# Optimization experiments

Measured on AMD Instinct MI355X. Metric: run time of the kernel, lower is better.

Reference implementation:

```python
import jax, jax.numpy as jnp
import numpy as np

G, B, DEG, BATCH = 4000, 8, 32, 128  # genes, per-gene layersize, off-diag blocks/gene, batch


def setup_inputs() -> dict:
    key = jax.random.key(0)
    rng = np.random.default_rng(0)
    # block structure: DEG off-diagonal PPI blocks per gene + reflexive diagonal
    src = np.repeat(np.arange(G, dtype=np.int32), DEG)
    off = 1 + rng.integers(0, G - 1, size=G * DEG)          # never 0 -> off-diagonal
    dst = ((src.astype(np.int64) + off) % G).astype(np.int32)
    diag = np.arange(G, dtype=np.int32)
    block_in = jnp.asarray(np.concatenate([src, diag]))      # [N] = [G*DEG + G]
    block_out = jnp.asarray(np.concatenate([dst, diag]))     # [N]
    n_blocks = G * DEG + G
    k1, k2 = jax.random.split(key)
    x = jax.random.normal(k1, (BATCH, G * B), dtype=jnp.float32)
    w = jax.random.normal(k2, (n_blocks, B, B), dtype=jnp.float32) * 0.05
    return {"x": x, "w": w, "block_in": block_in, "block_out": block_out}


def reference(x, w, block_in, block_out):
    batch, d = x.shape
    n_blocks, b, _ = w.shape
    g = d // b
    xb = x.reshape(batch, g, b)
    xin = xb[:, block_in, :]                        # [batch, N, b] irregular gather
    contrib = jnp.einsum('bni,nio->nbo', xin, w)    # [N, batch, b] tiny per-block GEMMs
    out = jax.ops.segment_sum(contrib, block_out, num_segments=g)  # [g, batch, b] scatter-add
    out = jnp.transpose(out, (1, 0, 2)).reshape(batch, d)
    # activation_function is identity (default lambda x: x); residual=True
    return out + x
```

## Files before the change

kernel.cpp:

```cpp
#include <hip/hip_runtime.h>
#include <hip/hip_bf16.h>

#define G      4000
#define DEG    32
#define BATCH  128
#define D      32000
#define NBLK   132000
#define ZBLK   NBLK
#define CAP    96

typedef __attribute__((ext_vector_type(8))) short bf16x8;
typedef __attribute__((ext_vector_type(4))) float f32x4;

__device__ inline unsigned bf16rne(float f) {
    unsigned u = __float_as_uint(f);
    return (u + 0x7fffu + ((u >> 16) & 1u)) >> 16;
}

__global__ void zero_cnt_kernel(int* cnt) {
    int i = blockIdx.x * 256 + threadIdx.x;
    if (i < G) cnt[i] = 0;
}

#define NB_BUILD 516
#define NB_TR    1000
#define NB_WP    4126

__global__ __launch_bounds__(256) void prep_kernel(const float* __restrict__ x,
                                                   const float* __restrict__ w,
                                                   const int* __restrict__ block_in,
                                                   const int* __restrict__ block_out,
                                                   int* __restrict__ cnt,
                                                   int2* __restrict__ pairs,
                                                   unsigned short* __restrict__ xgb,
                                                   unsigned short* __restrict__ wtb) {
    __shared__ float tile[32][132];
    const int bid = blockIdx.x;
    const int t   = threadIdx.x;

    if (bid < NB_BUILD) {
        int n = bid * 256 + t;
        if (n < NBLK) {
            int dst = block_out[n];
            int src = block_in[n];
            int pos = atomicAdd(&cnt[dst], 1);
            if (pos < CAP) pairs[dst * CAP + pos] = make_int2(n, src);
        }
    } else if (bid < NB_BUILD + NB_TR) {
        int id = bid - NB_BUILD;
        int c0 = (id % 250) * 128;
        int b0 = (id / 250) * 32;
#pragma unroll
        for (int it = 0; it < 4; ++it) {
            int l  = it * 1024 + t * 4;
            int br = l >> 7;
            int c  = l & 127;
            float4 v = *(const float4*)(x + (size_t)(b0 + br) * D + c0 + c);
            *(float4*)&tile[br][c] = v;
        }
        __syncthreads();
#pragma unroll
        for (int it = 0; it < 2; ++it) {
            int idx = it * 256 + t;
            int gl  = idx >> 5;
            int bl  = idx & 31;
            float4 v0 = *(const float4*)&tile[bl][gl * 8];
            float4 v1 = *(const float4*)&tile[bl][gl * 8 + 4];
            uint4 p;
            p.x = bf16rne(v0.x) | (bf16rne(v0.y) << 16);
            p.y = bf16rne(v0.z) | (bf16rne(v0.w) << 16);
            p.z = bf16rne(v1.x) | (bf16rne(v1.y) << 16);
            p.w = bf16rne(v1.z) | (bf16rne(v1.w) << 16);
            int gidx = (c0 >> 3) + gl;
            *(uint4*)(xgb + ((size_t)gidx * BATCH + b0 + bl) * 8) = p;
        }
    } else {
        int idx = (bid - (NB_BUILD + NB_TR)) * 256 + t;
        if (idx < (NBLK + 1) * 8) {
            int n = idx >> 3;
            int o = idx & 7;
            float v[8];
            if (n < NBLK) {
#pragma unroll
                for (int i = 0; i < 8; ++i) v[i] = w[(size_t)n * 64 + i * 8 + o];
            } else {
#pragma unroll
                for (int i = 0; i < 8; ++i) v[i] = 0.0f;
            }
            uint4 p;
            p.x = bf16rne(v[0]) | (bf16rne(v[1]) << 16);
            p.y = bf16rne(v[2]) | (bf16rne(v[3]) << 16);
            p.z = bf16rne(v[4]) | (bf16rne(v[5]) << 16);
            p.w = bf16rne(v[6]) | (bf16rne(v[7]) << 16);
            *(uint4*)(wtb + (size_t)n * 64 + o * 8) = p;
        }
    }
}

__global__ __launch_bounds__(256) void compute_kernel(const float* __restrict__ x,
                                                      const unsigned short* __restrict__ xgb,
                                                      const unsigned short* __restrict__ wtb,
                                                      const int2* __restrict__ pairs,
                                                      const int* __restrict__ cnt,
                                                      float* __restrict__ out) {
    const int g    = blockIdx.x;
    const int t    = threadIdx.x;
    const int wave = t >> 6;
    const int lane = t & 63;
    const int quad = lane >> 4;
    const int lo16 = lane & 15;

    __shared__ int sn[CAP];
    __shared__ int ss[CAP];

    int m = cnt[g];
    if (m > CAP) m = CAP;
    if (t < m) {
        int2 e = pairs[(size_t)g * CAP + t];
        sn[t] = e.x;
        ss[t] = e.y;
    }
    __syncthreads();

    const int    ob8   = (lo16 & 7) * 8;
    const int    mt0   = wave * 32 + lo16;
    const size_t a0off = (size_t)mt0 * 8;
    const size_t a1off = a0off + 128;

    f32x4 acc0 = {0.f, 0.f, 0.f, 0.f};
    f32x4 acc1 = {0.f, 0.f, 0.f, 0.f};

#define LOADSTEP(k0, A0, A1, BB)                                          \
    do {                                                                  \
        int kq_ = (k0) + quad;                                            \
        int v_  = kq_ < m;                                                \
        int kc_ = v_ ? kq_ : 0;                                           \
        int n_  = v_ ? sn[kc_] : ZBLK;                                    \
        int s_  = v_ ? ss[kc_] : 0;                                       \
        BB = *(const uint4*)(wtb + ((size_t)n_ << 6) + ob8);              \
        A0 = *(const uint4*)(xgb + ((size_t)s_ << 10) + a0off);           \
        A1 = *(const uint4*)(xgb + ((size_t)s_ << 10) + a1off);           \
    } while (0)

#define CONS(A0, A1, BB)                                                  \
    do {                                                                  \
        acc0 = __builtin_amdgcn_mfma_f32_16x16x32_bf16(                   \
            __builtin_bit_cast(bf16x8, A0), __builtin_bit_cast(bf16x8, BB), acc0, 0, 0, 0); \
        acc1 = __builtin_amdgcn_mfma_f32_16x16x32_bf16(                   \
            __builtin_bit_cast(bf16x8, A1), __builtin_bit_cast(bf16x8, BB), acc1, 0, 0, 0); \
    } while (0)

    uint4 Aa0, Aa1, Ab, Ba0, Ba1, Bb;

    LOADSTEP(0, Aa0, Aa1, Ab);
    for (int k0 = 0; k0 < m; k0 += 8) {
        LOADSTEP(k0 + 4, Ba0, Ba1, Bb);
        CONS(Aa0, Aa1, Ab);
        LOADSTEP(k0 + 8, Aa0, Aa1, Ab);
        CONS(Ba0, Ba1, Bb);
    }

    if (lo16 < 8) {
        const int col = g * 8 + lo16;
#pragma unroll
        for (int r = 0; r < 4; ++r) {
            int row0 = wave * 32 + quad * 4 + r;
            int row1 = row0 + 16;
            out[(size_t)row0 * D + col] = acc0[r] + x[(size_t)row0 * D + col];
            out[(size_t)row1 * D + col] = acc1[r] + x[(size_t)row1 * D + col];
        }
    }
#undef LOADSTEP
#undef CONS
}

extern "C" void kernel_launch(void* const* d_in, const int* in_sizes, int n_in,
                              void* d_out, int out_size, void* d_ws, size_t ws_size,
                              hipStream_t stream) {
    const float* x         = (const float*)d_in[0];
    const float* w         = (const float*)d_in[1];
    const int*   block_in  = (const int*)d_in[2];
    const int*   block_out = (const int*)d_in[3];
    float*       out       = (float*)d_out;

    char* ws = (char*)d_ws;
    int*            cnt   = (int*)ws;
    int2*           pairs = (int2*)(ws + 16384);
    unsigned short* xgb   = (unsigned short*)(ws + 3088384);
    unsigned short* wtb   = (unsigned short*)(ws + 11280384);

    zero_cnt_kernel<<<16, 256, 0, stream>>>(cnt);
    prep_kernel<<<NB_BUILD + NB_TR + NB_WP, 256, 0, stream>>>(x, w, block_in, block_out,
                                                              cnt, pairs, xgb, wtb);
    compute_kernel<<<G, 256, 0, stream>>>(x, xgb, wtb, pairs, cnt, out);
}
```

Measured before the change: 148.1 us.

## Coalesce weight transpose via LDS and deepen compute prefetch to four stages

The weight-prep branch now loads 64 blocks per workgroup with coalesced float4 reads into padded shared memory, then transposes and packs them to bf16. This replaces the strided per-element global reads and halves the number of prep workgroups. The compute kernel's gather loop moves from a two-stage to a four-stage register prefetch, which keeps more loads in flight at the cost of extra registers and more wasted zero-block loads past the end of the loop.

```diff
diff --git a/kernel.cpp b/kernel.cpp
--- a/kernel.cpp
+++ b/kernel.cpp
@@ -24,7 +24,7 @@
 
 #define NB_BUILD 516
 #define NB_TR    1000
-#define NB_WP    4126
+#define NB_W     2063
 
 __global__ __launch_bounds__(256) void prep_kernel(const float* __restrict__ x,
                                                    const float* __restrict__ w,
@@ -34,7 +34,7 @@
                                                    int2* __restrict__ pairs,
                                                    unsigned short* __restrict__ xgb,
                                                    unsigned short* __restrict__ wtb) {
-    __shared__ float tile[32][132];
+    __shared__ float shmem[64 * 68];
     const int bid = blockIdx.x;
     const int t   = threadIdx.x;
 
@@ -56,7 +56,7 @@
             int br = l >> 7;
             int c  = l & 127;
             float4 v = *(const float4*)(x + (size_t)(b0 + br) * D + c0 + c);
-            *(float4*)&tile[br][c] = v;
+            *(float4*)&shmem[br * 132 + c] = v;
         }
         __syncthreads();
 #pragma unroll
@@ -64,8 +64,8 @@
             int idx = it * 256 + t;
             int gl  = idx >> 5;
             int bl  = idx & 31;
-            float4 v0 = *(const float4*)&tile[bl][gl * 8];
-            float4 v1 = *(const float4*)&tile[bl][gl * 8 + 4];
+            float4 v0 = *(const float4*)&shmem[bl * 132 + gl * 8];
+            float4 v1 = *(const float4*)&shmem[bl * 132 + gl * 8 + 4];
             uint4 p;
             p.x = bf16rne(v0.x) | (bf16rne(v0.y) << 16);
             p.y = bf16rne(v0.z) | (bf16rne(v0.w) << 16);
@@ -75,24 +75,35 @@
             *(uint4*)(xgb + ((size_t)gidx * BATCH + b0 + bl) * 8) = p;
         }
     } else {
-        int idx = (bid - (NB_BUILD + NB_TR)) * 256 + t;
-        if (idx < (NBLK + 1) * 8) {
-            int n = idx >> 3;
-            int o = idx & 7;
-            float v[8];
-            if (n < NBLK) {
-#pragma unroll
-                for (int i = 0; i < 8; ++i) v[i] = w[(size_t)n * 64 + i * 8 + o];
-            } else {
-#pragma unroll
-                for (int i = 0; i < 8; ++i) v[i] = 0.0f;
+        int    id       = bid - (NB_BUILD + NB_TR);
+        size_t base_blk = (size_t)id * 64;
+        const float* wb = w + base_blk * 64;
+#pragma unroll
+        for (int j = 0; j < 4; ++j) {
+            int pos  = j * 1024 + t * 4;
+            int nl   = pos >> 6;
+            int rest = pos & 63;
+            float4 v;
+            if (base_blk + nl < NBLK) v = *(const float4*)(wb + pos);
+            else                      v = make_float4(0.f, 0.f, 0.f, 0.f);
+            *(float4*)&shmem[nl * 68 + rest] = v;
+        }
+        __syncthreads();
+#pragma unroll
+        for (int j = 0; j < 2; ++j) {
+            int p  = j * 256 + t;
+            int nl = p >> 3;
+            int o  = p & 7;
+            size_t nglob = base_blk + nl;
+            if (nglob <= NBLK) {
+                const float* r = &shmem[nl * 68 + o];
+                uint4 q;
+                q.x = bf16rne(r[0])  | (bf16rne(r[8])  << 16);
+                q.y = bf16rne(r[16]) | (bf16rne(r[24]) << 16);
+                q.z = bf16rne(r[32]) | (bf16rne(r[40]) << 16);
+                q.w = bf16rne(r[48]) | (bf16rne(r[56]) << 16);
+                *(uint4*)(wtb + nglob * 64 + o * 8) = q;
             }
-            uint4 p;
-            p.x = bf16rne(v[0]) | (bf16rne(v[1]) << 16);
-            p.y = bf16rne(v[2]) | (bf16rne(v[3]) << 16);
-            p.z = bf16rne(v[4]) | (bf16rne(v[5]) << 16);
-            p.w = bf16rne(v[6]) | (bf16rne(v[7]) << 16);
-            *(uint4*)(wtb + (size_t)n * 64 + o * 8) = p;
         }
     }
 }
@@ -150,14 +161,25 @@
             __builtin_bit_cast(bf16x8, A1), __builtin_bit_cast(bf16x8, BB), acc1, 0, 0, 0); \
     } while (0)
 
-    uint4 Aa0, Aa1, Ab, Ba0, Ba1, Bb;
-
-    LOADSTEP(0, Aa0, Aa1, Ab);
-    for (int k0 = 0; k0 < m; k0 += 8) {
-        LOADSTEP(k0 + 4, Ba0, Ba1, Bb);
-        CONS(Aa0, Aa1, Ab);
-        LOADSTEP(k0 + 8, Aa0, Aa1, Ab);
-        CONS(Ba0, Ba1, Bb);
+    uint4 Pa0, Pa1, Pb;
+    uint4 Qa0, Qa1, Qb;
+    uint4 Ra0, Ra1, Rb;
+    uint4 Sa0, Sa1, Sb;
+
+    LOADSTEP(0,  Pa0, Pa1, Pb);
+    LOADSTEP(4,  Qa0, Qa1, Qb);
+    LOADSTEP(8,  Ra0, Ra1, Rb);
+    LOADSTEP(12, Sa0, Sa1, Sb);
+
+    for (int k0 = 0; k0 < m; k0 += 16) {
+        CONS(Pa0, Pa1, Pb);
+        LOADSTEP(k0 + 16, Pa0, Pa1, Pb);
+        CONS(Qa0, Qa1, Qb);
+        LOADSTEP(k0 + 20, Qa0, Qa1, Qb);
+        CONS(Ra0, Ra1, Rb);
+        LOADSTEP(k0 + 24, Ra0, Ra1, Rb);
+        CONS(Sa0, Sa1, Sb);
+        LOADSTEP(k0 + 28, Sa0, Sa1, Sb);
     }
 
     if (lo16 < 8) {
@@ -190,7 +212,7 @@
     unsigned short* wtb   = (unsigned short*)(ws + 11280384);
 
     zero_cnt_kernel<<<16, 256, 0, stream>>>(cnt);
-    prep_kernel<<<NB_BUILD + NB_TR + NB_WP, 256, 0, stream>>>(x, w, block_in, block_out,
-                                                              cnt, pairs, xgb, wtb);
+    prep_kernel<<<NB_BUILD + NB_TR + NB_W, 256, 0, stream>>>(x, w, block_in, block_out,
+                                                             cnt, pairs, xgb, wtb);
     compute_kernel<<<G, 256, 0, stream>>>(x, xgb, wtb, pairs, cnt, out);
 }
```

After: 149.8 us. About the same (+1.2%).
